# Kernel tuning notes

Hardware: AMD Instinct MI355X
Metric: run time of the kernel (lower is better)

Reference implementation:

```python
import jax, jax.numpy as jnp
import numpy as np

N = 100_000       # nodes
E = 1_600_000     # edges (avg degree 16)
F_IN = 10         # num_node_features
H = 128           # hidden_dim
L = 3             # num_layers
G = 256           # number of graphs in the batch
C = 25            # num_classes
BN_EPS = 1e-5


def setup_inputs() -> dict:
    key = jax.random.key(0)
    ks = jax.random.split(key, 10)
    s = 0.05
    x = jax.random.normal(ks[0], (N, F_IN), dtype=jnp.float32)
    edge_index = jax.random.randint(ks[1], (2, E), 0, N, dtype=jnp.int32)
    batch = jnp.sort(jax.random.randint(ks[2], (N,), 0, G, dtype=jnp.int32))
    return {
        "x": x,
        "edge_index": edge_index,
        "batch": batch,
        "Wp": jax.random.normal(ks[3], (F_IN, H), dtype=jnp.float32) * s,
        "bp": jnp.zeros((H,), jnp.float32),
        "Wc": jax.random.normal(ks[4], (L, H, H), dtype=jnp.float32) * s,
        "bc": jnp.zeros((L, H), jnp.float32),
        "bn_gamma": jnp.ones((L, H), jnp.float32),
        "bn_beta": jnp.zeros((L, H), jnp.float32),
        "bn_mean": jax.random.normal(ks[5], (L, H), dtype=jnp.float32) * 0.1,
        "bn_var": jax.random.uniform(ks[6], (L, H), minval=0.5, maxval=1.5, dtype=jnp.float32),
        "W1": jax.random.normal(ks[7], (2 * H, H), dtype=jnp.float32) * s,
        "b1": jnp.zeros((H,), jnp.float32),
        "W2": jax.random.normal(ks[8], (H, C), dtype=jnp.float32) * s,
        "b2": jnp.zeros((C,), jnp.float32),
    }


def reference(x, edge_index, batch, Wp, bp, Wc, bc, bn_gamma, bn_beta,
              bn_mean, bn_var, W1, b1, W2, b2):
    n = x.shape[0]
    # GCNConv: add self loops, symmetric degree normalization (eval semantics:
    # batchnorm uses running stats, dropout is identity).
    loop = jnp.arange(n, dtype=edge_index.dtype)
    rows = jnp.concatenate([edge_index[0], loop])  # target / aggregation index
    cols = jnp.concatenate([edge_index[1], loop])  # source / gather index
    deg = jax.ops.segment_sum(jnp.ones_like(rows, dtype=x.dtype), rows, num_segments=n)
    dinv = jax.lax.rsqrt(deg)  # deg >= 1 thanks to self loops
    norm = dinv[rows] * dinv[cols]  # [E+N]

    h = jax.nn.relu(x @ Wp + bp)
    for i in range(L):
        hw = h @ Wc[i]                                   # [N, H]
        msg = hw[cols] * norm[:, None]                   # gather + scale
        agg = jax.ops.segment_sum(msg, rows, num_segments=n) + bc[i]
        bn = (agg - bn_mean[i]) * jax.lax.rsqrt(bn_var[i] + BN_EPS) * bn_gamma[i] + bn_beta[i]
        h = jax.nn.relu(bn)

    counts = jax.ops.segment_sum(jnp.ones((n,), h.dtype), batch, num_segments=G)
    x_mean = jax.ops.segment_sum(h, batch, num_segments=G) / jnp.maximum(counts, 1.0)[:, None]
    x_max = jax.ops.segment_max(h, batch, num_segments=G)
    x_max = jnp.where(counts[:, None] > 0, x_max, 0.0)   # guard empty graphs
    g = jnp.concatenate([x_mean, x_max], axis=1)          # [G, 2H]
    return jax.nn.relu(g @ W1 + b1) @ W2 + b2             # [G, C]
```

## Files before the change

### kernel.cpp

```cpp
#include <hip/hip_runtime.h>

#define N_NODES   100000
#define N_EDGES   1600000
#define F_IN      10
#define HD        128
#define N_LAYERS  3
#define N_GRAPHS  256
#define N_CLASSES 25
#define BN_EPS    1e-5f
#define POOL_TILE 64
#define LDS_PITCH 152

#define NBUCK     196
#define SCAT_TILE 4096
#define BUCK_CAP  16384

typedef __attribute__((ext_vector_type(8))) short bf8;
typedef __attribute__((ext_vector_type(4))) float f32x4;

static __device__ __forceinline__ unsigned short f2bf(float f){
    unsigned u = __float_as_uint(f);
    unsigned r = (u + 0x7fffu + ((u >> 16) & 1u)) >> 16;
    return (unsigned short)r;
}
static __device__ __forceinline__ float bflo(unsigned u){ return __uint_as_float(u << 16); }
static __device__ __forceinline__ float bfhi(unsigned u){ return __uint_as_float(u & 0xffff0000u); }
static __device__ __forceinline__ unsigned packbf(float a, float b){
    return (unsigned)f2bf(a) | ((unsigned)f2bf(b) << 16);
}


__global__ __launch_bounds__(256) void k_hist(const int* __restrict__ rows,
        int* __restrict__ gcount, int e){
    __shared__ int lhist[NBUCK];
    int t = threadIdx.x;
    if (t < NBUCK) lhist[t] = 0;
    __syncthreads();
    int i0 = blockIdx.x*SCAT_TILE + t;
    #pragma unroll
    for (int k = 0; k < 16; k++){
        int i = i0 + k*256;
        if (i < e) atomicAdd(&lhist[rows[i] >> 9], 1);
    }
    __syncthreads();
    if (t < NBUCK && lhist[t] > 0) atomicAdd(&gcount[t], lhist[t]);
}

__global__ void k_scanb(const int* __restrict__ gcount, int* __restrict__ base,
        int* __restrict__ cursor, int* __restrict__ rowptr, int e, int n){
    __shared__ int s[256];
    int t = threadIdx.x;
    int v = (t < NBUCK) ? gcount[t] : 0;
    s[t] = v;
    __syncthreads();
    for (int d = 1; d < 256; d <<= 1){
        int tv = (t >= d) ? s[t-d] : 0;
        __syncthreads();
        s[t] += tv;
        __syncthreads();
    }
    if (t < NBUCK){ base[t] = s[t] - v; cursor[t] = s[t] - v; }
    if (t == 0){ base[NBUCK] = e; rowptr[n] = e; }
}

__global__ __launch_bounds__(256) void k_scatter(const int* __restrict__ rows,
        const int* __restrict__ cols, int* __restrict__ cursor,
        unsigned* __restrict__ ebuf, int e){
    __shared__ int lbase[NBUCK];
    __shared__ int lcur[NBUCK];
    __shared__ int gbase[NBUCK];
    __shared__ int sbuf[256];
    __shared__ unsigned sedge[SCAT_TILE];
    __shared__ unsigned char sbuck[SCAT_TILE];
    int t = threadIdx.x;
    int i0 = blockIdx.x*SCAT_TILE + t;
    int r[16], c[16];
    if (t < NBUCK) lcur[t] = 0;
    __syncthreads();
    #pragma unroll
    for (int k = 0; k < 16; k++){
        int i = i0 + k*256;
        if (i < e){
            r[k] = rows[i]; c[k] = cols[i];
            atomicAdd(&lcur[r[k] >> 9], 1);
        } else r[k] = -1;
    }
    __syncthreads();
    int myc = (t < NBUCK) ? lcur[t] : 0;
    sbuf[t] = myc;
    __syncthreads();
    for (int d = 1; d < 256; d <<= 1){
        int tv = (t >= d) ? sbuf[t-d] : 0;
        __syncthreads();
        sbuf[t] += tv;
        __syncthreads();
    }
    if (t < NBUCK){
        lbase[t] = sbuf[t] - myc;
        lcur[t]  = sbuf[t] - myc;
        if (myc > 0) gbase[t] = atomicAdd(&cursor[t], myc);
    }
    __syncthreads();
    #pragma unroll
    for (int k = 0; k < 16; k++){
        if (r[k] >= 0){
            int bk = r[k] >> 9;
            int off = atomicAdd(&lcur[bk], 1);
            sedge[off] = ((unsigned)(r[k] & 511) << 17) | (unsigned)c[k];
            sbuck[off] = (unsigned char)bk;
        }
    }
    __syncthreads();
    int tot = sbuf[255];
    for (int i = t; i < tot; i += 256){
        int bk = sbuck[i];
        ebuf[gbase[bk] + (i - lbase[bk])] = sedge[i];
    }
}

__global__ __launch_bounds__(512) void k_build(const unsigned* __restrict__ ebuf,
        const int* __restrict__ base, int* __restrict__ rowptr,
        float* __restrict__ dinv, int* __restrict__ colidx, int n){
    __shared__ int hist[512];
    __shared__ int cur[512];
    __shared__ int colstage[BUCK_CAP];
    int b = blockIdx.x;
    int s = base[b], e = base[b+1];
    int cnt = e - s;
    int row0 = b << 9;
    int nrows = min(512, n - row0);
    int t = threadIdx.x;
    hist[t] = 0;
    __syncthreads();
    for (int i = t; i < cnt; i += 512)
        atomicAdd(&hist[ebuf[s + i] >> 17], 1);
    __syncthreads();
    int myc = hist[t];
    cur[t] = myc;
    __syncthreads();
    for (int d = 1; d < 512; d <<= 1){
        int tv = (t >= d) ? cur[t-d] : 0;
        __syncthreads();
        cur[t] += tv;
        __syncthreads();
    }
    int excl = cur[t] - myc;
    if (t < nrows){
        rowptr[row0 + t] = s + excl;
        dinv[row0 + t] = rsqrtf((float)(myc + 1));
    }
    cur[t] = excl;
    __syncthreads();
    for (int i = t; i < cnt; i += 512){
        unsigned v = ebuf[s + i];
        int off = atomicAdd(&cur[v >> 17], 1);
        colstage[off] = (int)(v & 0x1ffffu);
    }
    __syncthreads();
    for (int i = t; i < cnt; i += 512)
        colidx[s + i] = colstage[i];
}

__global__ void k_prepW(const float* __restrict__ Wc, unsigned short* __restrict__ WT){
    int i = blockIdx.x*256 + threadIdx.x;
    int l = i >> 14;
    int r = (i >> 7) & 127;
    int c = i & 127;
    WT[(l << 14) + c*HD + r] = f2bf(Wc[i]);
}

__global__ void k_proj(const float* __restrict__ x, const float* __restrict__ Wp,
                       const float* __restrict__ bp, unsigned* __restrict__ hbf, int n){
    __shared__ float sW[F_IN*HD];
    __shared__ float sb[HD];
    for (int t = threadIdx.x; t < F_IN*HD; t += 256) sW[t] = Wp[t];
    if (threadIdx.x < HD) sb[threadIdx.x] = bp[threadIdx.x];
    __syncthreads();
    int j  = threadIdx.x & 63;
    int ln = threadIdx.x >> 6;
    for (int n0 = blockIdx.x*4 + ln; n0 < n; n0 += gridDim.x*4){
        float a0 = sb[2*j], a1 = sb[2*j+1];
        #pragma unroll
        for (int k = 0; k < F_IN; k++){
            float xv = x[(size_t)n0*F_IN + k];
            a0 += xv * sW[k*HD + 2*j];
            a1 += xv * sW[k*HD + 2*j+1];
        }
        hbf[(size_t)n0*64 + j] = packbf(fmaxf(a0, 0.f), fmaxf(a1, 0.f));
    }
}

__global__ __launch_bounds__(256) void k_gemm(const unsigned short* __restrict__ hbf,
        const unsigned short* __restrict__ WT, const float* __restrict__ dinv,
        unsigned short* __restrict__ hw, int n){
    extern __shared__ char smem[];
    unsigned short* As = (unsigned short*)smem;
    unsigned short* Bs = As + 128*LDS_PITCH;
    int tid = threadIdx.x;
    int row0 = blockIdx.x * 128;

    const uint4* h4 = (const uint4*)hbf;
    const uint4* w4 = (const uint4*)WT;
    #pragma unroll
    for (int q = tid; q < 2048; q += 256){
        int r = q >> 4, c = q & 15;
        uint4 v = make_uint4(0u,0u,0u,0u);
        if (row0 + r < n) v = h4[(size_t)(row0 + r)*16 + c];
        *(uint4*)&As[r*LDS_PITCH + c*8] = v;
        *(uint4*)&Bs[r*LDS_PITCH + c*8] = w4[r*16 + c];
    }
    __syncthreads();

    int w = tid >> 6, lane = tid & 63;
    int l15 = lane & 15, quad = lane >> 4;
    f32x4 acc[2][8];
    #pragma unroll
    for (int rt = 0; rt < 2; rt++)
        #pragma unroll
        for (int ct = 0; ct < 8; ct++) acc[rt][ct] = (f32x4){0.f,0.f,0.f,0.f};

    int arow = w*32 + l15;
    #pragma unroll
    for (int kc = 0; kc < 4; kc++){
        int ko = kc*32 + quad*8;
        bf8 a0 = *(const bf8*)&As[arow*LDS_PITCH + ko];
        bf8 a1 = *(const bf8*)&As[(arow+16)*LDS_PITCH + ko];
        #pragma unroll
        for (int ct = 0; ct < 8; ct++){
            bf8 b = *(const bf8*)&Bs[(ct*16 + l15)*LDS_PITCH + ko];
            acc[0][ct] = __builtin_amdgcn_mfma_f32_16x16x32_bf16(a0, b, acc[0][ct], 0, 0, 0);
            acc[1][ct] = __builtin_amdgcn_mfma_f32_16x16x32_bf16(a1, b, acc[1][ct], 0, 0, 0);
        }
    }

    #pragma unroll
    for (int rt = 0; rt < 2; rt++){
        #pragma unroll
        for (int reg = 0; reg < 4; reg++){
            int row = row0 + w*32 + rt*16 + quad*4 + reg;
            if (row < n){
                float dv = dinv[row];
                #pragma unroll
                for (int ct = 0; ct < 8; ct++){
                    hw[(size_t)row*HD + ct*16 + l15] = f2bf(acc[rt][ct][reg] * dv);
                }
            }
        }
    }
}

__global__ __launch_bounds__(256) void k_agg(const unsigned* __restrict__ hw4,
        const int* __restrict__ rowptr, const int* __restrict__ colidx,
        const float* __restrict__ dinv, const float* __restrict__ bc,
        const float* __restrict__ bmean, const float* __restrict__ bvar,
        const float* __restrict__ bgamma, const float* __restrict__ bbeta,
        unsigned* __restrict__ houtb, float* __restrict__ hout32, int n){
    int node = blockIdx.x*4 + (threadIdx.x >> 6);
    int lane = threadIdx.x & 63;
    if (node >= n) return;
    unsigned self = hw4[(size_t)node*64 + lane];
    float ax = bflo(self), ay = bfhi(self);
    float bx = 0.f, by = 0.f;
    int s = rowptr[node], e = rowptr[node+1];
    int t = s;
    for (; t + 4 <= e; t += 4){
        int c0 = colidx[t],   c1 = colidx[t+1];
        int c2 = colidx[t+2], c3 = colidx[t+3];
        unsigned v0 = hw4[(size_t)c0*64 + lane];
        unsigned v1 = hw4[(size_t)c1*64 + lane];
        unsigned v2 = hw4[(size_t)c2*64 + lane];
        unsigned v3 = hw4[(size_t)c3*64 + lane];
        ax += bflo(v0); ay += bfhi(v0);
        bx += bflo(v1); by += bfhi(v1);
        ax += bflo(v2); ay += bfhi(v2);
        bx += bflo(v3); by += bfhi(v3);
    }
    for (; t < e; t++){
        unsigned v = hw4[(size_t)colidx[t]*64 + lane];
        ax += bflo(v); ay += bfhi(v);
    }
    ax += bx; ay += by;
    float dv = dinv[node];
    float2 cb  = ((const float2*)bc)[lane];
    float2 cm  = ((const float2*)bmean)[lane];
    float2 cv  = ((const float2*)bvar)[lane];
    float2 cg  = ((const float2*)bgamma)[lane];
    float2 cbe = ((const float2*)bbeta)[lane];
    float rx = (ax*dv + cb.x - cm.x) * rsqrtf(cv.x + BN_EPS) * cg.x + cbe.x;
    float ry = (ay*dv + cb.y - cm.y) * rsqrtf(cv.y + BN_EPS) * cg.y + cbe.y;
    rx = fmaxf(rx, 0.f); ry = fmaxf(ry, 0.f);
    houtb[(size_t)node*64 + lane] = packbf(rx, ry);
    if (hout32) ((float2*)hout32)[(size_t)node*64 + lane] = make_float2(rx, ry);
}

__global__ void k_count(const int* __restrict__ batch, int* __restrict__ gcnt, int n){
    int g = threadIdx.x;
    int lo = 0, hi = n;
    while (lo < hi){ int mid = (lo + hi) >> 1; if (batch[mid] < g) lo = mid + 1; else hi = mid; }
    int start = lo;
    hi = n;
    while (lo < hi){ int mid = (lo + hi) >> 1; if (batch[mid] < g + 1) lo = mid + 1; else hi = mid; }
    gcnt[g] = lo - start;
}

__global__ void k_pool(const float* __restrict__ h, const int* __restrict__ batch,
        float* __restrict__ gsum, int* __restrict__ gmax, int n){
    int f = threadIdx.x;
    int start = blockIdx.x * POOL_TILE;
    int end = min(start + POOL_TILE, n);
    if (start >= end) return;
    int cur = batch[start];
    float s = 0.f, mx = 0.f;
    for (int i = start; i < end; i++){
        int b = batch[i];
        float v = h[(size_t)i*HD + f];
        if (b != cur){
            atomicAdd(&gsum[cur*HD+f], s);
            atomicMax(&gmax[cur*HD+f], __float_as_int(mx));
            s = 0.f; mx = 0.f; cur = b;
        }
        s += v; mx = fmaxf(mx, v);
    }
    atomicAdd(&gsum[cur*HD+f], s);
    atomicMax(&gmax[cur*HD+f], __float_as_int(mx));
}

__global__ void k_mlp1(const float* __restrict__ gsum, const int* __restrict__ gmax,
        const int* __restrict__ gcnt, const float* __restrict__ W1,
        const float* __restrict__ b1, float* __restrict__ hidden){
    __shared__ float gv[2*HD];
    int g = blockIdx.x, j = threadIdx.x;
    float denom = (float)max(gcnt[g], 1);
    gv[j]    = gsum[g*HD+j] / denom;
    gv[HD+j] = __int_as_float(gmax[g*HD+j]);
    __syncthreads();
    float acc = b1[j];
    #pragma unroll 8
    for (int k = 0; k < 2*HD; k++) acc += gv[k]*W1[k*HD + j];
    hidden[g*HD + j] = fmaxf(acc, 0.f);
}

__global__ void k_mlp2(const float* __restrict__ hidden, const float* __restrict__ W2,
        const float* __restrict__ b2, float* __restrict__ out){
    int g = blockIdx.x, c = threadIdx.x;
    if (c >= N_CLASSES) return;
    float acc = b2[c];
    #pragma unroll 4
    for (int j = 0; j < HD; j++) acc += hidden[g*HD + j]*W2[j*N_CLASSES + c];
    out[g*N_CLASSES + c] = acc;
}

extern "C" void kernel_launch(void* const* d_in, const int* in_sizes, int n_in,
                              void* d_out, int out_size, void* d_ws, size_t ws_size,
                              hipStream_t stream){
    const float* x   = (const float*)d_in[0];
    const int*  eidx = (const int*)d_in[1];
    const int* batch = (const int*)d_in[2];
    const float* Wp  = (const float*)d_in[3];
    const float* bp  = (const float*)d_in[4];
    const float* Wc  = (const float*)d_in[5];
    const float* bc  = (const float*)d_in[6];
    const float* bng = (const float*)d_in[7];
    const float* bnb = (const float*)d_in[8];
    const float* bnm = (const float*)d_in[9];
    const float* bnv = (const float*)d_in[10];
    const float* W1  = (const float*)d_in[11];
    const float* b1  = (const float*)d_in[12];
    const float* W2  = (const float*)d_in[13];
    const float* b2  = (const float*)d_in[14];
    float* out = (float*)d_out;

    char* ws = (char*)d_ws;
    size_t off = 0;
    unsigned short* h_bf  = (unsigned short*)(ws + off); off += (size_t)N_NODES*HD*2;
    unsigned short* hw_bf = (unsigned short*)(ws + off); off += (size_t)N_NODES*HD*2;
    float* h32    = (float*)(ws + off); off += (size_t)N_NODES*HD*4;
    unsigned short* WT = (unsigned short*)(ws + off); off += (size_t)N_LAYERS*HD*HD*2;
    float* dinv   = (float*)(ws + off); off += (size_t)N_NODES*4;
    int*   rowptr = (int*)  (ws + off); off += (size_t)(N_NODES+16)*4;
    int*   colidx = (int*)  (ws + off); off += (size_t)N_EDGES*4;
    unsigned* ebuf= (unsigned*)(ws + off); off += (size_t)N_EDGES*4;
    int*   gcount = (int*)  (ws + off); off += 1024;
    int*   bbase  = (int*)  (ws + off); off += 1024;
    int*   bcur   = (int*)  (ws + off); off += 1024;
    float* gsum   = (float*)(ws + off); off += (size_t)N_GRAPHS*HD*4;
    int*   gmax   = (int*)  (ws + off); off += (size_t)N_GRAPHS*HD*4;
    int*   gcnt   = (int*)  (ws + off); off += 1024;
    float* hidden = (float*)(ws + off); off += (size_t)N_GRAPHS*HD*4;

    const int* rows = eidx;
    const int* cols = eidx + N_EDGES;

    hipMemsetAsync(gcount, 0, 1024, stream);
    hipMemsetAsync(gsum, 0, (size_t)(N_GRAPHS*HD*2)*4, stream);

    int nsb = (N_EDGES + SCAT_TILE - 1)/SCAT_TILE;
    k_hist   <<<nsb, 256, 0, stream>>>(rows, gcount, N_EDGES);
    k_scanb  <<<1, 256, 0, stream>>>(gcount, bbase, bcur, rowptr, N_EDGES, N_NODES);
    k_scatter<<<nsb, 256, 0, stream>>>(rows, cols, bcur, ebuf, N_EDGES);
    k_build  <<<NBUCK, 512, 0, stream>>>(ebuf, bbase, rowptr, dinv, colidx, N_NODES);

    k_prepW<<<(N_LAYERS*HD*HD)/256, 256, 0, stream>>>(Wc, WT);
    k_proj<<<1024, 256, 0, stream>>>(x, Wp, bp, (unsigned*)h_bf, N_NODES);

    int ntiles = (N_NODES + 127)/128;
    size_t shmem = (size_t)(2*128*LDS_PITCH)*2;
    for (int l = 0; l < N_LAYERS; l++){
        k_gemm<<<ntiles, 256, shmem, stream>>>(h_bf, WT + (size_t)l*HD*HD, dinv, hw_bf, N_NODES);
        k_agg<<<(N_NODES+3)/4, 256, 0, stream>>>((const unsigned*)hw_bf, rowptr, colidx, dinv,
            bc + l*HD, bnm + l*HD, bnv + l*HD, bng + l*HD, bnb + l*HD,
            (unsigned*)h_bf, (l == N_LAYERS-1) ? h32 : nullptr, N_NODES);
    }

    k_count<<<1, 256, 0, stream>>>(batch, gcnt, N_NODES);
    k_pool<<<(N_NODES+POOL_TILE-1)/POOL_TILE, 128, 0, stream>>>(h32, batch, gsum, gmax, N_NODES);
    k_mlp1<<<N_GRAPHS, 128, 0, stream>>>(gsum, gmax, gcnt, W1, b1, hidden);
    k_mlp2<<<N_GRAPHS, 32, 0, stream>>>(hidden, W2, b2, out);
}
```

Before: 479.2 us.

## Store node features in feature-chunked layout and aggregate per chunk

Node features and GEMM outputs move from row-major [N,128] bf16 to 8 column chunks of 16 features each ([chunk][N][16]). Aggregation is split across chunk-major blocks, and each wave handles 8 edges in parallel with 8 lanes per edge, then reduces with shuffles. The aim is to keep each chunk's 3.2 MB gather working set resident in cache and to raise memory-level parallelism per node. In exchange, the grid is 8x larger, colidx and rowptr are re-read once per chunk, and the GEMM loads and stores now touch scattered 32-byte segments.

New measurement: 1.245 ms. 2.6x slower.

```diff
diff --git a/kernel.cpp b/kernel.cpp
--- a/kernel.cpp
+++ b/kernel.cpp
@@ -14,6 +14,9 @@
 #define NBUCK     196
 #define SCAT_TILE 4096
 #define BUCK_CAP  16384
+
+#define NCHUNK    8
+#define AGG_BLKS  ((N_NODES + 3) / 4)
 
 typedef __attribute__((ext_vector_type(8))) short bf8;
 typedef __attribute__((ext_vector_type(4))) float f32x4;
@@ -170,7 +173,7 @@
 }
 
 __global__ void k_proj(const float* __restrict__ x, const float* __restrict__ Wp,
-                       const float* __restrict__ bp, unsigned* __restrict__ hbf, int n){
+                       const float* __restrict__ bp, unsigned* __restrict__ hC, int n){
     __shared__ float sW[F_IN*HD];
     __shared__ float sb[HD];
     for (int t = threadIdx.x; t < F_IN*HD; t += 256) sW[t] = Wp[t];
@@ -178,6 +181,7 @@
     __syncthreads();
     int j  = threadIdx.x & 63;
     int ln = threadIdx.x >> 6;
+    size_t cstride = (size_t)N_NODES*8;
     for (int n0 = blockIdx.x*4 + ln; n0 < n; n0 += gridDim.x*4){
         float a0 = sb[2*j], a1 = sb[2*j+1];
         #pragma unroll
@@ -186,26 +190,28 @@
             a0 += xv * sW[k*HD + 2*j];
             a1 += xv * sW[k*HD + 2*j+1];
         }
-        hbf[(size_t)n0*64 + j] = packbf(fmaxf(a0, 0.f), fmaxf(a1, 0.f));
-    }
-}
-
-__global__ __launch_bounds__(256) void k_gemm(const unsigned short* __restrict__ hbf,
+        hC[(size_t)(j >> 3)*cstride + (size_t)n0*8 + (j & 7)] =
+            packbf(fmaxf(a0, 0.f), fmaxf(a1, 0.f));
+    }
+}
+
+__global__ __launch_bounds__(256) void k_gemm(const unsigned* __restrict__ hC,
         const unsigned short* __restrict__ WT, const float* __restrict__ dinv,
-        unsigned short* __restrict__ hw, int n){
+        unsigned short* __restrict__ hwC, int n){
     extern __shared__ char smem[];
     unsigned short* As = (unsigned short*)smem;
     unsigned short* Bs = As + 128*LDS_PITCH;
     int tid = threadIdx.x;
     int row0 = blockIdx.x * 128;
 
-    const uint4* h4 = (const uint4*)hbf;
+    const uint4* h4 = (const uint4*)hC;
     const uint4* w4 = (const uint4*)WT;
     #pragma unroll
     for (int q = tid; q < 2048; q += 256){
         int r = q >> 4, c = q & 15;
+        int gr = row0 + r;
         uint4 v = make_uint4(0u,0u,0u,0u);
-        if (row0 + r < n) v = h4[(size_t)(row0 + r)*16 + c];
+        if (gr < n) v = h4[(size_t)(c >> 1)*(N_NODES*2) + (size_t)gr*2 + (c & 1)];
         *(uint4*)&As[r*LDS_PITCH + c*8] = v;
         *(uint4*)&Bs[r*LDS_PITCH + c*8] = w4[r*16 + c];
     }
@@ -242,55 +248,60 @@
                 float dv = dinv[row];
                 #pragma unroll
                 for (int ct = 0; ct < 8; ct++){
-                    hw[(size_t)row*HD + ct*16 + l15] = f2bf(acc[rt][ct][reg] * dv);
+                    hwC[(size_t)ct*(N_NODES*16) + (size_t)row*16 + l15] =
+                        f2bf(acc[rt][ct][reg] * dv);
                 }
             }
         }
     }
 }
 
-__global__ __launch_bounds__(256) void k_agg(const unsigned* __restrict__ hw4,
+__global__ __launch_bounds__(256) void k_agg(const unsigned* __restrict__ hwC,
         const int* __restrict__ rowptr, const int* __restrict__ colidx,
         const float* __restrict__ dinv, const float* __restrict__ bc,
         const float* __restrict__ bmean, const float* __restrict__ bvar,
         const float* __restrict__ bgamma, const float* __restrict__ bbeta,
-        unsigned* __restrict__ houtb, float* __restrict__ hout32, int n){
-    int node = blockIdx.x*4 + (threadIdx.x >> 6);
+        unsigned* __restrict__ houtC, float* __restrict__ hout32, int n){
+    int chunk = blockIdx.x / AGG_BLKS;
+    int nb    = blockIdx.x - chunk*AGG_BLKS;
+    int node = nb*4 + (threadIdx.x >> 6);
     int lane = threadIdx.x & 63;
     if (node >= n) return;
-    unsigned self = hw4[(size_t)node*64 + lane];
-    float ax = bflo(self), ay = bfhi(self);
-    float bx = 0.f, by = 0.f;
+    const unsigned* hw = hwC + (size_t)chunk*(N_NODES*8);
+    int g = lane >> 3, q = lane & 7;
+
+    float a0 = 0.f, a1 = 0.f;
+    if (g == 0){
+        unsigned sv = hw[(size_t)node*8 + q];
+        a0 = bflo(sv); a1 = bfhi(sv);
+    }
     int s = rowptr[node], e = rowptr[node+1];
-    int t = s;
-    for (; t + 4 <= e; t += 4){
-        int c0 = colidx[t],   c1 = colidx[t+1];
-        int c2 = colidx[t+2], c3 = colidx[t+3];
-        unsigned v0 = hw4[(size_t)c0*64 + lane];
-        unsigned v1 = hw4[(size_t)c1*64 + lane];
-        unsigned v2 = hw4[(size_t)c2*64 + lane];
-        unsigned v3 = hw4[(size_t)c3*64 + lane];
-        ax += bflo(v0); ay += bfhi(v0);
-        bx += bflo(v1); by += bfhi(v1);
-        ax += bflo(v2); ay += bfhi(v2);
-        bx += bflo(v3); by += bfhi(v3);
-    }
-    for (; t < e; t++){
-        unsigned v = hw4[(size_t)colidx[t]*64 + lane];
-        ax += bflo(v); ay += bfhi(v);
-    }
-    ax += bx; ay += by;
-    float dv = dinv[node];
-    float2 cb  = ((const float2*)bc)[lane];
-    float2 cm  = ((const float2*)bmean)[lane];
-    float2 cv  = ((const float2*)bvar)[lane];
-    float2 cg  = ((const float2*)bgamma)[lane];
-    float2 cbe = ((const float2*)bbeta)[lane];
-    float rx = (ax*dv + cb.x - cm.x) * rsqrtf(cv.x + BN_EPS) * cg.x + cbe.x;
-    float ry = (ay*dv + cb.y - cm.y) * rsqrtf(cv.y + BN_EPS) * cg.y + cbe.y;
-    rx = fmaxf(rx, 0.f); ry = fmaxf(ry, 0.f);
-    houtb[(size_t)node*64 + lane] = packbf(rx, ry);
-    if (hout32) ((float2*)hout32)[(size_t)node*64 + lane] = make_float2(rx, ry);
+    for (int t = s; t < e; t += 8){
+        int idx = t + g;
+        if (idx < e){
+            int col = colidx[idx];
+            unsigned v = hw[(size_t)col*8 + q];
+            a0 += bflo(v); a1 += bfhi(v);
+        }
+    }
+    a0 += __shfl_xor(a0, 8);  a1 += __shfl_xor(a1, 8);
+    a0 += __shfl_xor(a0, 16); a1 += __shfl_xor(a1, 16);
+    a0 += __shfl_xor(a0, 32); a1 += __shfl_xor(a1, 32);
+
+    if (lane < 8){
+        float dv = dinv[node];
+        int fp = chunk*8 + lane;
+        float2 cb  = ((const float2*)bc)[fp];
+        float2 cm  = ((const float2*)bmean)[fp];
+        float2 cv  = ((const float2*)bvar)[fp];
+        float2 cg  = ((const float2*)bgamma)[fp];
+        float2 cbe = ((const float2*)bbeta)[fp];
+        float rx = (a0*dv + cb.x - cm.x) * rsqrtf(cv.x + BN_EPS) * cg.x + cbe.x;
+        float ry = (a1*dv + cb.y - cm.y) * rsqrtf(cv.y + BN_EPS) * cg.y + cbe.y;
+        rx = fmaxf(rx, 0.f); ry = fmaxf(ry, 0.f);
+        houtC[(size_t)chunk*(N_NODES*8) + (size_t)node*8 + lane] = packbf(rx, ry);
+        if (hout32) ((float2*)hout32)[(size_t)node*64 + fp] = make_float2(rx, ry);
+    }
 }
 
 __global__ void k_count(const int* __restrict__ batch, int* __restrict__ gcnt, int n){
@@ -372,8 +383,8 @@
 
     char* ws = (char*)d_ws;
     size_t off = 0;
-    unsigned short* h_bf  = (unsigned short*)(ws + off); off += (size_t)N_NODES*HD*2;
-    unsigned short* hw_bf = (unsigned short*)(ws + off); off += (size_t)N_NODES*HD*2;
+    unsigned* hC   = (unsigned*)(ws + off); off += (size_t)N_NODES*HD*2;
+    unsigned short* hwC = (unsigned short*)(ws + off); off += (size_t)N_NODES*HD*2;
     float* h32    = (float*)(ws + off); off += (size_t)N_NODES*HD*4;
     unsigned short* WT = (unsigned short*)(ws + off); off += (size_t)N_LAYERS*HD*HD*2;
     float* dinv   = (float*)(ws + off); off += (size_t)N_NODES*4;
@@ -401,15 +412,15 @@
     k_build  <<<NBUCK, 512, 0, stream>>>(ebuf, bbase, rowptr, dinv, colidx, N_NODES);
 
     k_prepW<<<(N_LAYERS*HD*HD)/256, 256, 0, stream>>>(Wc, WT);
-    k_proj<<<1024, 256, 0, stream>>>(x, Wp, bp, (unsigned*)h_bf, N_NODES);
+    k_proj<<<1024, 256, 0, stream>>>(x, Wp, bp, hC, N_NODES);
 
     int ntiles = (N_NODES + 127)/128;
     size_t shmem = (size_t)(2*128*LDS_PITCH)*2;
     for (int l = 0; l < N_LAYERS; l++){
-        k_gemm<<<ntiles, 256, shmem, stream>>>(h_bf, WT + (size_t)l*HD*HD, dinv, hw_bf, N_NODES);
-        k_agg<<<(N_NODES+3)/4, 256, 0, stream>>>((const unsigned*)hw_bf, rowptr, colidx, dinv,
+        k_gemm<<<ntiles, 256, shmem, stream>>>(hC, WT + (size_t)l*HD*HD, dinv, hwC, N_NODES);
+        k_agg<<<NCHUNK*AGG_BLKS, 256, 0, stream>>>((const unsigned*)hwC, rowptr, colidx, dinv,
             bc + l*HD, bnm + l*HD, bnv + l*HD, bng + l*HD, bnb + l*HD,
-            (unsigned*)h_bf, (l == N_LAYERS-1) ? h32 : nullptr, N_NODES);
+            hC, (l == N_LAYERS-1) ? h32 : nullptr, N_NODES);
     }
 
     k_count<<<1, 256, 0, stream>>>(batch, gcnt, N_NODES);
```
